# Performance work log

Hardware: AMD Instinct MI355X
Metric: run time of the kernel (lower is better)

Reference implementation:

```python
import jax, jax.numpy as jnp
import numpy as np

D = 1024
H = 16
HD = D // H
EPS = 1e-5


def layer_norm(x, g, b):
    mu = jnp.mean(x, axis=-1, keepdims=True)
    var = jnp.mean((x - mu) ** 2, axis=-1, keepdims=True)
    return (x - mu) * jax.lax.rsqrt(var + EPS) * g + b


def setup_inputs() -> dict:
    key = jax.random.key(0)
    ks = jax.random.split(key, 10)
    s = lambda fan_in: 1.0 / np.sqrt(fan_in)
    inp = {
        "x": jax.random.normal(ks[0], (2, 2048, D), dtype=jnp.float32),
        "w_qkv": jax.random.uniform(ks[1], (D, 3 * D), minval=-s(D), maxval=s(D)),
        "b_qkv": jnp.zeros((3 * D,), jnp.float32),
        "w_fc": jax.random.uniform(ks[2], (D, D), minval=-s(D), maxval=s(D)),
        "b_fc": jnp.zeros((D,), jnp.float32),
        "ln1_g": jnp.ones((D,), jnp.float32),
        "ln1_b": jnp.zeros((D,), jnp.float32),
        "ln2_g": jnp.ones((D,), jnp.float32),
        "ln2_b": jnp.zeros((D,), jnp.float32),
        "w1": jax.random.uniform(ks[3], (D, 4 * D), minval=-s(D), maxval=s(D)),
        "b1": jnp.zeros((4 * D,), jnp.float32),
        "w2": jax.random.uniform(ks[4], (4 * D, D), minval=-s(4 * D), maxval=s(4 * D)),
        "b2": jnp.zeros((D,), jnp.float32),
    }
    return inp


def reference(x, w_qkv, b_qkv, w_fc, b_fc, ln1_g, ln1_b, ln2_g, ln2_b, w1, b1, w2, b2):
    B, T, C = x.shape
    # --- attention sublayer (pre-norm) ---
    h = layer_norm(x, ln1_g, ln1_b)
    qkv = (h @ w_qkv + b_qkv).reshape(B, T, 3, H, HD)
    q, k, v = qkv[:, :, 0], qkv[:, :, 1], qkv[:, :, 2]  # [B,T,H,HD]
    scores = jnp.einsum("bqhd,bkhd->bhqk", q, k) / np.sqrt(HD).astype(np.float32)
    causal = jnp.tril(jnp.ones((T, T), dtype=bool))
    scores = jnp.where(causal, scores, -jnp.inf)
    weights = jax.nn.softmax(scores, axis=-1)
    out = jnp.einsum("bhqk,bkhd->bqhd", weights, v).reshape(B, T, C)
    x = x + out @ w_fc + b_fc
    # --- MLP sublayer (pre-norm) ---
    h = layer_norm(x, ln2_g, ln2_b)
    h = jax.nn.gelu(h @ w1 + b1, approximate=False) @ w2 + b2
    return x + h
```

## Files before the change

### kernel.cpp

```cpp
#include <hip/hip_runtime.h>
#include <hip/hip_bf16.h>
#include <cstdint>
#include <cstddef>

#define SEQ 2048
#define DM  1024

typedef __attribute__((ext_vector_type(8))) __bf16 bf16x8;
typedef __attribute__((ext_vector_type(4))) float  f32x4;
using bf16 = __hip_bfloat16;

__device__ __forceinline__ void gload_lds16(const bf16* g, bf16* l) {
  __builtin_amdgcn_global_load_lds((const __attribute__((address_space(1))) void*)g,
                                   (__attribute__((address_space(3))) void*)l,
                                   16, 0, 0);
}

__global__ void transpose_to_bf16(const float* __restrict__ in, bf16* __restrict__ out,
                                  int K, int N) {
  __shared__ float tile[32][33];
  const int k0 = blockIdx.y * 32, n0 = blockIdx.x * 32;
  const int tx = threadIdx.x, ty = threadIdx.y;
#pragma unroll
  for (int i = ty; i < 32; i += 8)
    tile[i][tx] = in[(size_t)(k0 + i) * N + n0 + tx];
  __syncthreads();
#pragma unroll
  for (int i = ty; i < 32; i += 8)
    out[(size_t)(n0 + i) * K + k0 + tx] = __float2bfloat16(tile[tx][i]);
}

__global__ void ln_to_bf16(const float* __restrict__ x, const float* __restrict__ g,
                           const float* __restrict__ bt, bf16* __restrict__ out) {
  const int row = blockIdx.x;
  const float4 v = ((const float4*)(x + (size_t)row * DM))[threadIdx.x];
  float s  = v.x + v.y + v.z + v.w;
  float s2 = v.x * v.x + v.y * v.y + v.z * v.z + v.w * v.w;
#pragma unroll
  for (int o = 32; o > 0; o >>= 1) { s += __shfl_down(s, o); s2 += __shfl_down(s2, o); }
  __shared__ float red[8];
  const int wave = threadIdx.x >> 6, lane = threadIdx.x & 63;
  if (lane == 0) { red[wave] = s; red[4 + wave] = s2; }
  __syncthreads();
  s  = red[0] + red[1] + red[2] + red[3];
  s2 = red[4] + red[5] + red[6] + red[7];
  const float mu  = s * (1.f / DM);
  const float var = s2 * (1.f / DM) - mu * mu;
  const float r   = rsqrtf(var + 1e-5f);
  const float4 gv = ((const float4*)g)[threadIdx.x];
  const float4 bv = ((const float4*)bt)[threadIdx.x];
  bf16* o = out + (size_t)row * DM + threadIdx.x * 4;
  o[0] = __float2bfloat16((v.x - mu) * r * gv.x + bv.x);
  o[1] = __float2bfloat16((v.y - mu) * r * gv.y + bv.y);
  o[2] = __float2bfloat16((v.z - mu) * r * gv.z + bv.z);
  o[3] = __float2bfloat16((v.w - mu) * r * gv.w + bv.w);
}

enum { EP_BF16 = 0, EP_GELU = 1, EP_RESID = 2, EP_QKV = 3 };

template <int MODE, int TM, int TN>
__global__ void gemm_bt(const bf16* __restrict__ A, const bf16* __restrict__ Bt,
                        const float* __restrict__ bias, const float* __restrict__ resid,
                        float* __restrict__ Cf, bf16* __restrict__ Cb, bf16* __restrict__ vt,
                        int M, int N, int K) {
  constexpr int ABUF = TM * 32;
  constexpr int BBUF = TN * 32;
  constexpr int MI = TM / 32;
  constexpr int NI = TN / 32;
  __shared__ __attribute__((aligned(16))) bf16 As[2 * ABUF];
  __shared__ __attribute__((aligned(16))) bf16 Bs[2 * BBUF];
  const int tid  = threadIdx.x;
  const int wave = tid >> 6, lane = tid & 63;
  const int l16 = lane & 15, lq = lane >> 4;
  const int m0 = blockIdx.x * TM, n0 = blockIdx.y * TN;
  const int wr = (wave >> 1) * (TM / 2), wc = (wave & 1) * (TN / 2);

  f32x4 acc[MI][NI];
#pragma unroll
  for (int i = 0; i < MI; i++)
#pragma unroll
    for (int j = 0; j < NI; j++) acc[i][j] = 0;

  const int srow = tid >> 2;
  const int scol = (tid & 3) * 8;
  const bf16* ga = A  + (size_t)(m0 + srow) * K + scol;
  const bf16* gb = Bt + (size_t)(n0 + srow) * K + scol;

  {
    bf16* la = As + wave * 512;
    bf16* lb = Bs + wave * 512;
    gload_lds16(ga, la);
    if (TM == 128) gload_lds16(ga + (size_t)64 * K, la + 2048);
    gload_lds16(gb, lb);
    if (TN == 128) gload_lds16(gb + (size_t)64 * K, lb + 2048);
  }

  const int NKT = K >> 5;
  for (int it = 0; it < NKT; ++it) {
    __syncthreads();
    const int cur = it & 1, nxt = cur ^ 1;
    if (it + 1 < NKT) {
      const int kt = (it + 1) << 5;
      bf16* la = As + nxt * ABUF + wave * 512;
      bf16* lb = Bs + nxt * BBUF + wave * 512;
      gload_lds16(ga + kt, la);
      if (TM == 128) gload_lds16(ga + (size_t)64 * K + kt, la + 2048);
      gload_lds16(gb + kt, lb);
      if (TN == 128) gload_lds16(gb + (size_t)64 * K + kt, lb + 2048);
    }
    bf16x8 af[MI], bfr[NI];
#pragma unroll
    for (int mi = 0; mi < MI; mi++)
      af[mi] = *(const bf16x8*)(As + cur * ABUF + (wr + mi * 16 + l16) * 32 + lq * 8);
#pragma unroll
    for (int ni = 0; ni < NI; ni++)
      bfr[ni] = *(const bf16x8*)(Bs + cur * BBUF + (wc + ni * 16 + l16) * 32 + lq * 8);
#pragma unroll
    for (int mi = 0; mi < MI; mi++)
#pragma unroll
      for (int ni = 0; ni < NI; ni++)
        acc[mi][ni] = __builtin_amdgcn_mfma_f32_16x16x32_bf16(af[mi], bfr[ni], acc[mi][ni], 0, 0, 0);
  }

#pragma unroll
  for (int ni = 0; ni < NI; ni++) {
    const int col = n0 + wc + ni * 16 + l16;
    const float bb = bias[col];
#pragma unroll
    for (int mi = 0; mi < MI; mi++) {
      if constexpr (MODE == EP_QKV) {
        const int row0 = m0 + wr + mi * 16 + lq * 4;
        if (col >= 2048) {
          __attribute__((aligned(8))) bf16 pk[4];
#pragma unroll
          for (int r = 0; r < 4; r++) pk[r] = __float2bfloat16(acc[mi][ni][r] + bb);
          *(uint2*)(vt + (size_t)((row0 >> 11) * 1024 + (col - 2048)) * SEQ + (row0 & 2047)) =
              *(const uint2*)pk;
        } else {
#pragma unroll
          for (int r = 0; r < 4; r++)
            Cb[(size_t)(row0 + r) * N + col] = __float2bfloat16(acc[mi][ni][r] + bb);
        }
      } else {
#pragma unroll
        for (int r = 0; r < 4; r++) {
          const int row = m0 + wr + mi * 16 + lq * 4 + r;
          const size_t idx = (size_t)row * N + col;
          float v = acc[mi][ni][r] + bb;
          if (MODE == EP_BF16) {
            Cb[idx] = __float2bfloat16(v);
          } else if (MODE == EP_GELU) {
            v = 0.5f * v * (1.0f + erff(v * 0.70710678118654752f));
            Cb[idx] = __float2bfloat16(v);
          } else {
            Cf[idx] = resid[idx] + v;
          }
        }
      }
    }
  }
}

__global__ __launch_bounds__(256, 4)
void gemm_bt64(const bf16* __restrict__ A, const bf16* __restrict__ Bt,
               const float* __restrict__ bias, const float* __restrict__ resid,
               float* __restrict__ Cf, int M, int N, int K) {
  constexpr int TILE = 64 * 64;
  __shared__ __attribute__((aligned(16))) bf16 As[2 * TILE];
  __shared__ __attribute__((aligned(16))) bf16 Bs[2 * TILE];
  const int tid  = threadIdx.x;
  const int wave = tid >> 6, lane = tid & 63;
  const int l16 = lane & 15, lq = lane >> 4;
  const int m0 = blockIdx.x * 64, n0 = blockIdx.y * 64;
  const int wr = (wave >> 1) * 32, wc = (wave & 1) * 32;

  f32x4 acc[2][2];
#pragma unroll
  for (int i = 0; i < 2; i++)
#pragma unroll
    for (int j = 0; j < 2; j++) acc[i][j] = 0;

  const int srow = tid >> 3;
  const int scb  = (tid & 7) ^ (srow & 7);
  const bf16* ga0 = A  + (size_t)(m0 + srow) * K + scb * 8;
  const bf16* ga1 = A  + (size_t)(m0 + srow + 32) * K + scb * 8;
  const bf16* gb0 = Bt + (size_t)(n0 + srow) * K + scb * 8;
  const bf16* gb1 = Bt + (size_t)(n0 + srow + 32) * K + scb * 8;
  const int ld0 = wave * 512;
  const int ld1 = 2048 + wave * 512;

  gload_lds16(ga0, As + ld0);
  gload_lds16(ga1, As + ld1);
  gload_lds16(gb0, Bs + ld0);
  gload_lds16(gb1, Bs + ld1);

  const int sxa = l16 & 7;

  const int NKT = K >> 6;
  for (int it = 0; it < NKT; ++it) {
    __syncthreads();
    const int cur = (it & 1) * TILE;
    if (it + 1 < NKT) {
      const int nxt = ((it + 1) & 1) * TILE;
      const int kt = (it + 1) << 6;
      gload_lds16(ga0 + kt, As + nxt + ld0);
      gload_lds16(ga1 + kt, As + nxt + ld1);
      gload_lds16(gb0 + kt, Bs + nxt + ld0);
      gload_lds16(gb1 + kt, Bs + nxt + ld1);
    }
    bf16x8 af[2][2], bfv[2][2];
#pragma unroll
    for (int mi = 0; mi < 2; mi++) {
      const int row = wr + mi * 16 + l16;
#pragma unroll
      for (int kk = 0; kk < 2; kk++)
        af[mi][kk] = *(const bf16x8*)(As + cur + row * 64 + (((kk * 4 + lq) ^ sxa) << 3));
    }
#pragma unroll
    for (int ni = 0; ni < 2; ni++) {
      const int row = wc + ni * 16 + l16;
#pragma unroll
      for (int kk = 0; kk < 2; kk++)
        bfv[ni][kk] = *(const bf16x8*)(Bs + cur + row * 64 + (((kk * 4 + lq) ^ sxa) << 3));
    }
#pragma unroll
    for (int kk = 0; kk < 2; kk++)
#pragma unroll
      for (int mi = 0; mi < 2; mi++)
#pragma unroll
        for (int ni = 0; ni < 2; ni++)
          acc[mi][ni] = __builtin_amdgcn_mfma_f32_16x16x32_bf16(af[mi][kk], bfv[ni][kk],
                                                                acc[mi][ni], 0, 0, 0);
  }

#pragma unroll
  for (int ni = 0; ni < 2; ni++) {
    const int col = n0 + wc + ni * 16 + l16;
    const float bb = bias[col];
#pragma unroll
    for (int mi = 0; mi < 2; mi++) {
#pragma unroll
      for (int r = 0; r < 4; r++) {
        const int row = m0 + wr + mi * 16 + lq * 4 + r;
        const size_t idx = (size_t)row * N + col;
        Cf[idx] = resid[idx] + acc[mi][ni][r] + bb;
      }
    }
  }
}

#define SCALE_LOG2 0.18033688011112042f

__global__ __launch_bounds__(256, 4)
void flash_attn(const bf16* __restrict__ qkv, const bf16* __restrict__ VTg,
                bf16* __restrict__ out) {
  const int id = blockIdx.x;
  const int a  = id & 7;
  const int h  = (id >> 3) & 15;
  const int b  = (id >> 7) & 1;
  const int m  = (id >> 8) & 3;
  const int qb = a ^ (((m & 1) * 15) | ((m & 2) << 3));

  const int tid = threadIdx.x;
  const int w = tid >> 6, lane = tid & 63;
  const int l16 = lane & 15, lq = lane >> 4;

  const size_t base = (size_t)b * SEQ * 3072;
  const bf16* Qg = qkv + base + (size_t)h * 64;
  const bf16* Kg = qkv + base + 1024 + (size_t)h * 64;
  const bf16* Vt = VTg + (size_t)(b * 1024 + h * 64) * SEQ;

  __shared__ __attribute__((aligned(16))) bf16 Ks[2 * 4096];
  __shared__ __attribute__((aligned(16))) bf16 VTs[2 * 4096];
  __shared__ __attribute__((aligned(16))) bf16 Ps[4 * 1024];

  const int q0 = qb * 64;
  const int nkb = qb + 1;

  const int srow = tid >> 3;
  const int scb  = (tid & 7) ^ (srow & 7);
  const bf16* gK0 = Kg + (size_t)srow * 3072 + scb * 8;
  const bf16* gK1 = Kg + (size_t)(srow + 32) * 3072 + scb * 8;
  const bf16* gV0 = Vt + (size_t)srow * SEQ + scb * 8;
  const bf16* gV1 = Vt + (size_t)(srow + 32) * SEQ + scb * 8;
  const int ldst0 = w * 512;
  const int ldst1 = 2048 + w * 512;

  gload_lds16(gK0, Ks + ldst0);
  gload_lds16(gK1, Ks + ldst1);
  gload_lds16(gV0, VTs + ldst0);
  gload_lds16(gV1, VTs + ldst1);

  const bf16* qrow = Qg + (size_t)(q0 + w * 16 + l16) * 3072 + lq * 8;
  const bf16x8 qf0 = *(const bf16x8*)(qrow);
  const bf16x8 qf1 = *(const bf16x8*)(qrow + 32);

  const int koffA = l16 * 64 + ((lq ^ (l16 & 7)) << 3);
  const int koffB = l16 * 64 + (((4 + lq) ^ (l16 & 7)) << 3);
  const int l16h = l16 >> 3;
  const int pco  = w * 1024 + (l16 & 7);

  f32x4 oacc[4];
#pragma unroll
  for (int i = 0; i < 4; i++) oacc[i] = 0;
  float lsum[4] = {0.f, 0.f, 0.f, 0.f};

  for (int kb = 0; kb < nkb; ++kb) {
    __syncthreads();
    const int cur = (kb & 1) * 4096;
    if (kb + 1 < nkb) {
      const int nxt = ((kb + 1) & 1) * 4096;
      const size_t ko = (size_t)(kb + 1) * 64;
      gload_lds16(gK0 + ko * 3072, Ks + nxt + ldst0);
      gload_lds16(gK1 + ko * 3072, Ks + nxt + ldst1);
      gload_lds16(gV0 + ko, VTs + nxt + ldst0);
      gload_lds16(gV1 + ko, VTs + nxt + ldst1);
    }

    f32x4 sacc[4];
#pragma unroll
    for (int nt = 0; nt < 4; nt++) sacc[nt] = 0;
#pragma unroll
    for (int nt = 0; nt < 4; nt++) {
      const bf16x8 kf0 = *(const bf16x8*)(Ks + cur + nt * 1024 + koffA);
      const bf16x8 kf1 = *(const bf16x8*)(Ks + cur + nt * 1024 + koffB);
      sacc[nt] = __builtin_amdgcn_mfma_f32_16x16x32_bf16(qf0, kf0, sacc[nt], 0, 0, 0);
      sacc[nt] = __builtin_amdgcn_mfma_f32_16x16x32_bf16(qf1, kf1, sacc[nt], 0, 0, 0);
    }

    if (kb == qb) {
#pragma unroll
      for (int r = 0; r < 4; r++) {
        const int rowp = lq * 4 + r;
        const int qloc = w * 16 + rowp;
        float e[4];
#pragma unroll
        for (int nt = 0; nt < 4; nt++) {
          float sv = sacc[nt][r] * SCALE_LOG2;
          sv = fminf(sv, 88.f);
          if (nt * 16 + l16 > qloc) sv = -1e30f;
          e[nt] = exp2f(sv);
          Ps[pco + rowp * 64 + ((((nt * 2 + l16h)) ^ (rowp & 7)) << 3)] = __float2bfloat16(e[nt]);
        }
        lsum[r] += (e[0] + e[1]) + (e[2] + e[3]);
      }
    } else {
#pragma unroll
      for (int r = 0; r < 4; r++) {
        const int rowp = lq * 4 + r;
        float e[4];
#pragma unroll
        for (int nt = 0; nt < 4; nt++) {
          float sv = sacc[nt][r] * SCALE_LOG2;
          sv = fminf(sv, 88.f);
          e[nt] = exp2f(sv);
          Ps[pco + rowp * 64 + ((((nt * 2 + l16h)) ^ (rowp & 7)) << 3)] = __float2bfloat16(e[nt]);
        }
        lsum[r] += (e[0] + e[1]) + (e[2] + e[3]);
      }
    }

    const bf16x8 pf0 = *(const bf16x8*)(Ps + w * 1024 + koffA);
    const bf16x8 pf1 = *(const bf16x8*)(Ps + w * 1024 + koffB);
#pragma unroll
    for (int dt = 0; dt < 4; dt++) {
      const bf16x8 vf0 = *(const bf16x8*)(VTs + cur + dt * 1024 + koffA);
      const bf16x8 vf1 = *(const bf16x8*)(VTs + cur + dt * 1024 + koffB);
      oacc[dt] = __builtin_amdgcn_mfma_f32_16x16x32_bf16(pf0, vf0, oacc[dt], 0, 0, 0);
      oacc[dt] = __builtin_amdgcn_mfma_f32_16x16x32_bf16(pf1, vf1, oacc[dt], 0, 0, 0);
    }
  }

#pragma unroll
  for (int r = 0; r < 4; r++) {
    float l = lsum[r];
    l += __shfl_xor(l, 1);
    l += __shfl_xor(l, 2);
    l += __shfl_xor(l, 4);
    l += __shfl_xor(l, 8);
    lsum[r] = 1.f / l;
  }
#pragma unroll
  for (int dt = 0; dt < 4; dt++)
#pragma unroll
    for (int r = 0; r < 4; r++) {
      const int qrow_ = q0 + w * 16 + lq * 4 + r;
      const float v = oacc[dt][r] * lsum[r];
      out[(size_t)(b * SEQ + qrow_) * DM + h * 64 + dt * 16 + l16] = __float2bfloat16(v);
    }
}

extern "C" void kernel_launch(void* const* d_in, const int* in_sizes, int n_in,
                              void* d_out, int out_size, void* d_ws, size_t ws_size,
                              hipStream_t stream) {
  const float* x     = (const float*)d_in[0];
  const float* w_qkv = (const float*)d_in[1];
  const float* b_qkv = (const float*)d_in[2];
  const float* w_fc  = (const float*)d_in[3];
  const float* b_fc  = (const float*)d_in[4];
  const float* ln1_g = (const float*)d_in[5];
  const float* ln1_b = (const float*)d_in[6];
  const float* ln2_g = (const float*)d_in[7];
  const float* ln2_b = (const float*)d_in[8];
  const float* w1    = (const float*)d_in[9];
  const float* b1    = (const float*)d_in[10];
  const float* w2    = (const float*)d_in[11];
  const float* b2    = (const float*)d_in[12];
  float* out = (float*)d_out;

  char* ws    = (char*)d_ws;
  float* x2   = (float*)(ws);
  bf16* VTg   = (bf16*)(ws);
  bf16* big   = (bf16*)(ws + (size_t)(16 << 20));
  bf16* small = (bf16*)(ws + (size_t)(48 << 20));
  bf16* wT    = (bf16*)(ws + (size_t)(56 << 20));

  const dim3 tb(32, 8);

  ln_to_bf16<<<dim3(4096), dim3(256), 0, stream>>>(x, ln1_g, ln1_b, small);
  transpose_to_bf16<<<dim3(96, 32), tb, 0, stream>>>(w_qkv, wT, 1024, 3072);
  gemm_bt<EP_QKV, 128, 128><<<dim3(32, 24), dim3(256), 0, stream>>>(
      small, wT, b_qkv, nullptr, nullptr, big, VTg, 4096, 3072, 1024);
  flash_attn<<<dim3(1024), dim3(256), 0, stream>>>(big, VTg, small);
  transpose_to_bf16<<<dim3(32, 32), tb, 0, stream>>>(w_fc, wT, 1024, 1024);
  gemm_bt64<<<dim3(64, 16), dim3(256), 0, stream>>>(
      small, wT, b_fc, x, x2, 4096, 1024, 1024);
  ln_to_bf16<<<dim3(4096), dim3(256), 0, stream>>>(x2, ln2_g, ln2_b, small);
  transpose_to_bf16<<<dim3(128, 32), tb, 0, stream>>>(w1, wT, 1024, 4096);
  gemm_bt<EP_GELU, 128, 128><<<dim3(32, 32), dim3(256), 0, stream>>>(
      small, wT, b1, nullptr, nullptr, big, nullptr, 4096, 4096, 1024);
  transpose_to_bf16<<<dim3(32, 128), tb, 0, stream>>>(w2, wT, 4096, 1024);
  gemm_bt64<<<dim3(64, 16), dim3(256), 0, stream>>>(
      big, wT, b2, x2, out, 4096, 1024, 4096);
}
```

Before: 354.2 us.

## Pair complementary causal query blocks in one 512-thread attention workgroup

Each attention workgroup now has 8 waves and handles two query blocks, p and 31-p. Both halves share the K/V tiles streamed into LDS, which halves K/V global traffic and balances causal work across workgroups. The cost is that waves for the low block sit idle once they pass their diagonal but still hit every barrier, and the larger 512-thread blocks lower occupancy flexibility.

```diff
diff --git a/kernel.cpp b/kernel.cpp
--- a/kernel.cpp
+++ b/kernel.cpp
@@ -251,19 +251,22 @@
 
 #define SCALE_LOG2 0.18033688011112042f
 
-__global__ __launch_bounds__(256, 4)
+__global__ __launch_bounds__(512, 2)
 void flash_attn(const bf16* __restrict__ qkv, const bf16* __restrict__ VTg,
                 bf16* __restrict__ out) {
-  const int id = blockIdx.x;
-  const int a  = id & 7;
-  const int h  = (id >> 3) & 15;
-  const int b  = (id >> 7) & 1;
-  const int m  = (id >> 8) & 3;
-  const int qb = a ^ (((m & 1) * 15) | ((m & 2) << 3));
+  const int idx  = blockIdx.x;
+  const int praw = idx & 15;
+  const int p    = ((idx >> 8) & 1) ? (15 - praw) : praw;
+  const int bh   = (idx >> 4) & 31;
+  const int h    = bh & 15;
+  const int b    = bh >> 4;
+  const int qlow = p, qhigh = 31 - p;
 
   const int tid = threadIdx.x;
   const int w = tid >> 6, lane = tid & 63;
+  const int wq = w & 3, hf = w >> 2;
   const int l16 = lane & 15, lq = lane >> 4;
+  const int myqb = hf ? qlow : qhigh;
 
   const size_t base = (size_t)b * SEQ * 3072;
   const bf16* Qg = qkv + base + (size_t)h * 64;
@@ -272,26 +275,18 @@
 
   __shared__ __attribute__((aligned(16))) bf16 Ks[2 * 4096];
   __shared__ __attribute__((aligned(16))) bf16 VTs[2 * 4096];
-  __shared__ __attribute__((aligned(16))) bf16 Ps[4 * 1024];
-
-  const int q0 = qb * 64;
-  const int nkb = qb + 1;
+  __shared__ __attribute__((aligned(16))) bf16 Ps[8 * 1024];
 
   const int srow = tid >> 3;
   const int scb  = (tid & 7) ^ (srow & 7);
-  const bf16* gK0 = Kg + (size_t)srow * 3072 + scb * 8;
-  const bf16* gK1 = Kg + (size_t)(srow + 32) * 3072 + scb * 8;
-  const bf16* gV0 = Vt + (size_t)srow * SEQ + scb * 8;
-  const bf16* gV1 = Vt + (size_t)(srow + 32) * SEQ + scb * 8;
-  const int ldst0 = w * 512;
-  const int ldst1 = 2048 + w * 512;
-
-  gload_lds16(gK0, Ks + ldst0);
-  gload_lds16(gK1, Ks + ldst1);
-  gload_lds16(gV0, VTs + ldst0);
-  gload_lds16(gV1, VTs + ldst1);
-
-  const bf16* qrow = Qg + (size_t)(q0 + w * 16 + l16) * 3072 + lq * 8;
+  const bf16* gK = Kg + (size_t)srow * 3072 + scb * 8;
+  const bf16* gV = Vt + (size_t)srow * SEQ + scb * 8;
+  const int ldst = w * 512;
+
+  gload_lds16(gK, Ks + ldst);
+  gload_lds16(gV, VTs + ldst);
+
+  const bf16* qrow = Qg + (size_t)(myqb * 64 + wq * 16 + l16) * 3072 + lq * 8;
   const bf16x8 qf0 = *(const bf16x8*)(qrow);
   const bf16x8 qf1 = *(const bf16x8*)(qrow + 32);
 
@@ -305,69 +300,70 @@
   for (int i = 0; i < 4; i++) oacc[i] = 0;
   float lsum[4] = {0.f, 0.f, 0.f, 0.f};
 
-  for (int kb = 0; kb < nkb; ++kb) {
+  const int nkt = qhigh + 1;
+  for (int kb = 0; kb < nkt; ++kb) {
     __syncthreads();
     const int cur = (kb & 1) * 4096;
-    if (kb + 1 < nkb) {
+    if (kb + 1 < nkt) {
       const int nxt = ((kb + 1) & 1) * 4096;
       const size_t ko = (size_t)(kb + 1) * 64;
-      gload_lds16(gK0 + ko * 3072, Ks + nxt + ldst0);
-      gload_lds16(gK1 + ko * 3072, Ks + nxt + ldst1);
-      gload_lds16(gV0 + ko, VTs + nxt + ldst0);
-      gload_lds16(gV1 + ko, VTs + nxt + ldst1);
-    }
-
-    f32x4 sacc[4];
-#pragma unroll
-    for (int nt = 0; nt < 4; nt++) sacc[nt] = 0;
-#pragma unroll
-    for (int nt = 0; nt < 4; nt++) {
-      const bf16x8 kf0 = *(const bf16x8*)(Ks + cur + nt * 1024 + koffA);
-      const bf16x8 kf1 = *(const bf16x8*)(Ks + cur + nt * 1024 + koffB);
-      sacc[nt] = __builtin_amdgcn_mfma_f32_16x16x32_bf16(qf0, kf0, sacc[nt], 0, 0, 0);
-      sacc[nt] = __builtin_amdgcn_mfma_f32_16x16x32_bf16(qf1, kf1, sacc[nt], 0, 0, 0);
-    }
-
-    if (kb == qb) {
-#pragma unroll
-      for (int r = 0; r < 4; r++) {
-        const int rowp = lq * 4 + r;
-        const int qloc = w * 16 + rowp;
-        float e[4];
-#pragma unroll
-        for (int nt = 0; nt < 4; nt++) {
-          float sv = sacc[nt][r] * SCALE_LOG2;
-          sv = fminf(sv, 88.f);
-          if (nt * 16 + l16 > qloc) sv = -1e30f;
-          e[nt] = exp2f(sv);
-          Ps[pco + rowp * 64 + ((((nt * 2 + l16h)) ^ (rowp & 7)) << 3)] = __float2bfloat16(e[nt]);
+      gload_lds16(gK + ko * 3072, Ks + nxt + ldst);
+      gload_lds16(gV + ko, VTs + nxt + ldst);
+    }
+
+    if (kb <= myqb) {
+      f32x4 sacc[4];
+#pragma unroll
+      for (int nt = 0; nt < 4; nt++) sacc[nt] = 0;
+#pragma unroll
+      for (int nt = 0; nt < 4; nt++) {
+        const bf16x8 kf0 = *(const bf16x8*)(Ks + cur + nt * 1024 + koffA);
+        const bf16x8 kf1 = *(const bf16x8*)(Ks + cur + nt * 1024 + koffB);
+        sacc[nt] = __builtin_amdgcn_mfma_f32_16x16x32_bf16(qf0, kf0, sacc[nt], 0, 0, 0);
+        sacc[nt] = __builtin_amdgcn_mfma_f32_16x16x32_bf16(qf1, kf1, sacc[nt], 0, 0, 0);
+      }
+
+      if (kb == myqb) {
+#pragma unroll
+        for (int r = 0; r < 4; r++) {
+          const int rowp = lq * 4 + r;
+          const int qloc = wq * 16 + rowp;
+          float e[4];
+#pragma unroll
+          for (int nt = 0; nt < 4; nt++) {
+            float sv = sacc[nt][r] * SCALE_LOG2;
+            sv = fminf(sv, 88.f);
+            if (nt * 16 + l16 > qloc) sv = -1e30f;
+            e[nt] = exp2f(sv);
+            Ps[pco + rowp * 64 + ((((nt * 2 + l16h)) ^ (rowp & 7)) << 3)] = __float2bfloat16(e[nt]);
+          }
+          lsum[r] += (e[0] + e[1]) + (e[2] + e[3]);
         }
-        lsum[r] += (e[0] + e[1]) + (e[2] + e[3]);
+      } else {
+#pragma unroll
+        for (int r = 0; r < 4; r++) {
+          const int rowp = lq * 4 + r;
+          float e[4];
+#pragma unroll
+          for (int nt = 0; nt < 4; nt++) {
+            float sv = sacc[nt][r] * SCALE_LOG2;
+            sv = fminf(sv, 88.f);
+            e[nt] = exp2f(sv);
+            Ps[pco + rowp * 64 + ((((nt * 2 + l16h)) ^ (rowp & 7)) << 3)] = __float2bfloat16(e[nt]);
+          }
+          lsum[r] += (e[0] + e[1]) + (e[2] + e[3]);
+        }
       }
-    } else {
-#pragma unroll
-      for (int r = 0; r < 4; r++) {
-        const int rowp = lq * 4 + r;
-        float e[4];
-#pragma unroll
-        for (int nt = 0; nt < 4; nt++) {
-          float sv = sacc[nt][r] * SCALE_LOG2;
-          sv = fminf(sv, 88.f);
-          e[nt] = exp2f(sv);
-          Ps[pco + rowp * 64 + ((((nt * 2 + l16h)) ^ (rowp & 7)) << 3)] = __float2bfloat16(e[nt]);
-        }
-        lsum[r] += (e[0] + e[1]) + (e[2] + e[3]);
+
+      const bf16x8 pf0 = *(const bf16x8*)(Ps + w * 1024 + koffA);
+      const bf16x8 pf1 = *(const bf16x8*)(Ps + w * 1024 + koffB);
+#pragma unroll
+      for (int dt = 0; dt < 4; dt++) {
+        const bf16x8 vf0 = *(const bf16x8*)(VTs + cur + dt * 1024 + koffA);
+        const bf16x8 vf1 = *(const bf16x8*)(VTs + cur + dt * 1024 + koffB);
+        oacc[dt] = __builtin_amdgcn_mfma_f32_16x16x32_bf16(pf0, vf0, oacc[dt], 0, 0, 0);
+        oacc[dt] = __builtin_amdgcn_mfma_f32_16x16x32_bf16(pf1, vf1, oacc[dt], 0, 0, 0);
       }
-    }
-
-    const bf16x8 pf0 = *(const bf16x8*)(Ps + w * 1024 + koffA);
-    const bf16x8 pf1 = *(const bf16x8*)(Ps + w * 1024 + koffB);
-#pragma unroll
-    for (int dt = 0; dt < 4; dt++) {
-      const bf16x8 vf0 = *(const bf16x8*)(VTs + cur + dt * 1024 + koffA);
-      const bf16x8 vf1 = *(const bf16x8*)(VTs + cur + dt * 1024 + koffB);
-      oacc[dt] = __builtin_amdgcn_mfma_f32_16x16x32_bf16(pf0, vf0, oacc[dt], 0, 0, 0);
-      oacc[dt] = __builtin_amdgcn_mfma_f32_16x16x32_bf16(pf1, vf1, oacc[dt], 0, 0, 0);
     }
   }
 
@@ -384,7 +380,7 @@
   for (int dt = 0; dt < 4; dt++)
 #pragma unroll
     for (int r = 0; r < 4; r++) {
-      const int qrow_ = q0 + w * 16 + lq * 4 + r;
+      const int qrow_ = myqb * 64 + wq * 16 + lq * 4 + r;
       const float v = oacc[dt][r] * lsum[r];
       out[(size_t)(b * SEQ + qrow_) * DM + h * 64 + dt * 16 + l16] = __float2bfloat16(v);
     }
@@ -421,7 +417,7 @@
   transpose_to_bf16<<<dim3(96, 32), tb, 0, stream>>>(w_qkv, wT, 1024, 3072);
   gemm_bt<EP_QKV, 128, 128><<<dim3(32, 24), dim3(256), 0, stream>>>(
       small, wT, b_qkv, nullptr, nullptr, big, VTg, 4096, 3072, 1024);
-  flash_attn<<<dim3(1024), dim3(256), 0, stream>>>(big, VTg, small);
+  flash_attn<<<dim3(512), dim3(512), 0, stream>>>(big, VTg, small);
   transpose_to_bf16<<<dim3(32, 32), tb, 0, stream>>>(w_fc, wT, 1024, 1024);
   gemm_bt64<<<dim3(64, 16), dim3(256), 0, stream>>>(
       small, wT, b_fc, x, x2, 4096, 1024, 1024);
```

Result: no change. 351.7 us (-0.7%).
